# Optimization experiments

Hardware: AMD Instinct MI355X
Metric: run time of the kernel (lower is better)

Reference implementation:

```python
import jax, jax.numpy as jnp
import numpy as np

N, C = 8192, 256
CQK = C // 8  # q/k projection dim = 32


def setup_inputs() -> dict:
    key = jax.random.key(0)
    k1, k2, k3, k4, k5 = jax.random.split(key, 5)
    f = jax.random.normal(k1, (N, C), dtype=jnp.float32)
    Wqk = jax.random.normal(k2, (CQK, C), dtype=jnp.float32) * (1.0 / np.sqrt(C))
    Wv = jax.random.normal(k3, (C, C), dtype=jnp.float32) * (1.0 / np.sqrt(C))
    bv = jax.random.normal(k4, (C,), dtype=jnp.float32) * 0.01
    gamma = jax.random.normal(k5, (1,), dtype=jnp.float32)
    return {"f": f, "Wqk": Wqk, "Wv": Wv, "bv": bv, "gamma": gamma}


def reference(f, Wqk, Wv, bv, gamma):
    # f: [N, C] point features. 1x1 convs over the point dim == per-point linear.
    q = f @ Wqk.T                      # [N, CQK] (q and k share weights)
    # energy[i, j] = <q_i, k_j>; q == k here, no 1/sqrt(d) scaling (faithful)
    energy = q @ q.T                   # [N, N]
    attn = jax.nn.softmax(energy, axis=-1)  # softmax over last dim (dim=-1)
    v = f @ Wv.T + bv                  # [N, C]
    # torch: bmm(x_v [1,C,N], attn [1,N,N]) -> out[c, j] = sum_i v[i, c] * attn[i, j]
    attn_out = jnp.einsum('ij,ic->jc', attn, v)  # [N, C]
    return gamma[0] * attn_out + f     # [N, C]
```

## Files before the change

kernel.cpp:

```cpp
#include <hip/hip_runtime.h>
#include <hip/hip_bf16.h>

#define NN 8192
#define CC 256
#define CQK 32
#define JS 4

using bf16x8 = __attribute__((ext_vector_type(8))) short;
using f16x8  = __attribute__((ext_vector_type(8))) _Float16;
using s16x4  = __attribute__((ext_vector_type(4))) short;
using f32x4  = __attribute__((ext_vector_type(4))) float;
using f32x16 = __attribute__((ext_vector_type(16))) float;

static __device__ __forceinline__ unsigned short f2bf(float x) {
    union { __hip_bfloat16 h; unsigned short u; } cv;
    cv.h = __float2bfloat16(x);
    return cv.u;
}
static __device__ __forceinline__ float fexp2(float x) { return __builtin_amdgcn_exp2f(x); }
static __device__ __forceinline__ int packbf(float lo, float hi) {
    union { float f; unsigned u; } a, b;
    a.f = lo; b.f = hi;
    return (int)((b.u & 0xFFFF0000u) | (a.u >> 16));
}

__global__ __launch_bounds__(256) void conv_w_kernel(
    const float* __restrict__ Wv, unsigned short* __restrict__ WvB)
{
    const int idx = (blockIdx.x * 256 + threadIdx.x) * 4;
    float4 v = *(const float4*)(Wv + idx);
    s16x4 pk;
    pk[0] = (short)f2bf(v.x); pk[1] = (short)f2bf(v.y);
    pk[2] = (short)f2bf(v.z); pk[3] = (short)f2bf(v.w);
    *(s16x4*)(WvB + idx) = pk;
}

__global__ __launch_bounds__(256) void proj_q_kernel(
    const float* __restrict__ f, const float* __restrict__ Wqk,
    unsigned short* __restrict__ qf)
{
    __shared__ __align__(16) float fl[8][CC];
    const int t  = threadIdx.x;
    const int r0 = blockIdx.x * 8;
    {
        const float4* src = (const float4*)(f + (size_t)r0 * CC);
        float4* dst = (float4*)&fl[0][0];
        dst[t]       = src[t];
        dst[t + 256] = src[t + 256];
    }
    __syncthreads();
    const int cq = t & 31;
    const int rg = t >> 5;
    const float4* w4 = (const float4*)(Wqk + (size_t)cq * CC);
    float a = 0.f;
    for (int k4 = 0; k4 < 64; ++k4) {
        float4 wq = w4[k4];
        const float4 fv = *(const float4*)&fl[rg][k4 * 4];
        a = fmaf(wq.x, fv.x, a);
        a = fmaf(wq.y, fv.y, a);
        a = fmaf(wq.z, fv.z, a);
        a = fmaf(wq.w, fv.w, a);
    }
    a *= 1.2011224087864498f;
    union { _Float16 h; unsigned short u; } cv;
    cv.h = (_Float16)a;
    qf[(size_t)(r0 + rg) * CQK + cq] = cv.u;
}

__global__ __launch_bounds__(256, 4) void proj_v_kernel(
    const float* __restrict__ f, const unsigned short* __restrict__ WvB,
    const float* __restrict__ bv, unsigned short* __restrict__ vB)
{
    const int t    = threadIdx.x;
    const int lane = t & 63;
    const int w    = t >> 6;
    const int l31  = lane & 31;
    const int h    = lane >> 5;
    const int nb   = blockIdx.x * 32;
    const int cb   = w * 64;

    f32x16 acc[2];
#pragma unroll
    for (int cf = 0; cf < 2; ++cf)
#pragma unroll
        for (int r = 0; r < 16; ++r) acc[cf][r] = 0.f;

    const float* frow = f + (size_t)(nb + l31) * CC;
#pragma unroll
    for (int ks = 0; ks < 16; ++ks) {
        const int k0 = ks * 16 + 8 * h;
        float4 a0 = *(const float4*)(frow + k0);
        float4 a1 = *(const float4*)(frow + k0 + 4);
        bf16x8 af;
        af[0] = (short)f2bf(a0.x); af[1] = (short)f2bf(a0.y);
        af[2] = (short)f2bf(a0.z); af[3] = (short)f2bf(a0.w);
        af[4] = (short)f2bf(a1.x); af[5] = (short)f2bf(a1.y);
        af[6] = (short)f2bf(a1.z); af[7] = (short)f2bf(a1.w);
#pragma unroll
        for (int cf = 0; cf < 2; ++cf) {
            const bf16x8 bw = *(const bf16x8*)(WvB + (size_t)(cb + 32 * cf + l31) * CC + k0);
            acc[cf] = __builtin_amdgcn_mfma_f32_32x32x16_bf16(af, bw, acc[cf], 0, 0, 0);
        }
    }
#pragma unroll
    for (int cf = 0; cf < 2; ++cf) {
        const int cg = cb + 32 * cf + l31;
        const float bvc = bv[cg];
#pragma unroll
        for (int rg = 0; rg < 4; ++rg) {
            const int ib = (nb >> 3) + rg;
            s16x4 pk;
#pragma unroll
            for (int r = 0; r < 4; ++r)
                pk[r] = (short)f2bf(acc[cf][4 * rg + r] + bvc);
            *(s16x4*)(vB + ((size_t)ib * CC + cg) * 8 + 4 * h) = pk;
        }
    }
}

__global__ __launch_bounds__(256, 4) void pass1_kernel(
    const unsigned short* __restrict__ qf,
    float* __restrict__ ps)
{
    const int t    = threadIdx.x;
    const int lane = t & 63;
    const int w    = t >> 6;
    const int l31  = lane & 31;
    const int h    = lane >> 5;
    const int i0   = (blockIdx.x & 255) * 32;
    const int js   = blockIdx.x >> 8;
    const int JCH  = NN / JS / 4;
    const int jbase = js * (NN / JS) + w * JCH;

    const size_t qir = (size_t)(i0 + l31) * CQK;
    const f16x8 bi0 = *(const f16x8*)(qf + qir + 8 * h);
    const f16x8 bi1 = *(const f16x8*)(qf + qir + 16 + 8 * h);

    float s = 0.f;

#pragma unroll 2
    for (int st = 0; st < JCH; st += 32) {
        const size_t qjr = (size_t)(jbase + st + l31) * CQK;
        const f16x8 aj0 = *(const f16x8*)(qf + qjr + 8 * h);
        const f16x8 aj1 = *(const f16x8*)(qf + qjr + 16 + 8 * h);
        f32x16 ee = {0,0,0,0,0,0,0,0,0,0,0,0,0,0,0,0};
        ee = __builtin_amdgcn_mfma_f32_32x32x16_f16(aj0, bi0, ee, 0, 0, 0);
        ee = __builtin_amdgcn_mfma_f32_32x32x16_f16(aj1, bi1, ee, 0, 0, 0);
        float a_ = 0.f;
#pragma unroll
        for (int r = 0; r < 16; ++r) a_ += fexp2(ee[r]);
        s += a_;
    }
    s += __shfl_xor(s, 32);

    __shared__ float rs[4][32];
    if (lane < 32) rs[w][l31] = s;
    __syncthreads();
    if (t < 32) {
        float sf = rs[0][t] + rs[1][t] + rs[2][t] + rs[3][t];
        ps[(size_t)js * NN + i0 + t] = sf;
    }
}

__global__ __launch_bounds__(256) void finalize_kernel(
    const float* __restrict__ ps, float* __restrict__ bias)
{
    int i = blockIdx.x * 256 + threadIdx.x;
    float s = ps[i];
#pragma unroll
    for (int k = 1; k < JS; ++k) s += ps[(size_t)k * NN + i];
    bias[i] = __builtin_amdgcn_logf(s);
}

#define LOADQF(A0, A1, NI)                                                     \
    {                                                                          \
        const size_t qnr = (size_t)((NI) + l31) * CQK;                         \
        A0 = *(const f16x8*)(qf + qnr + 8 * h);                                \
        A1 = *(const f16x8*)(qf + qnr + 16 + 8 * h);                           \
    }

#define LOADVF2(VF, I)                                                         \
    _Pragma("unroll")                                                          \
    for (int s2 = 0; s2 < 2; ++s2)                                             \
        _Pragma("unroll")                                                      \
        for (int cf = 0; cf < 4; ++cf)                                         \
            VF[s2][cf] = *(const bf16x8*)(                                     \
                vB + ((size_t)(((I) >> 3) + 2 * s2 + h) * CC + cb + 32 * cf + l31) * 8);

#define LOADB42(B4, I)                                                         \
    _Pragma("unroll")                                                          \
    for (int rg = 0; rg < 4; ++rg)                                             \
        B4[rg] = *(const f32x4*)(bias + (I) + 8 * rg + 4 * h);

#define ECOMPF(EE, A0, A1)                                                     \
    {                                                                          \
        f32x16 z_ = {0,0,0,0,0,0,0,0,0,0,0,0,0,0,0,0};                         \
        z_ = __builtin_amdgcn_mfma_f32_32x32x16_f16(A1, bj1, z_, 0, 0, 0);     \
        EE = __builtin_amdgcn_mfma_f32_32x32x16_f16(A0, bj0, z_, 0, 0, 0);     \
    }

#define FINISH2(EE, B4, VF)                                                    \
    {                                                                          \
        int d0[4], d1[4];                                                      \
        _Pragma("unroll")                                                      \
        for (int rg = 0; rg < 4; ++rg) {                                       \
            float p0 = fexp2(EE[4 * rg + 0] - B4[rg][0]);                      \
            float p1 = fexp2(EE[4 * rg + 1] - B4[rg][1]);                      \
            float p2 = fexp2(EE[4 * rg + 2] - B4[rg][2]);                      \
            float p3 = fexp2(EE[4 * rg + 3] - B4[rg][3]);                      \
            d0[rg] = packbf(p0, p1);                                           \
            d1[rg] = packbf(p2, p3);                                           \
        }                                                                      \
        _Pragma("unroll")                                                      \
        for (int s2 = 0; s2 < 2; ++s2) {                                       \
            const int a_ = d0[2 * s2], b_ = d0[2 * s2 + 1];                    \
            const int c_ = d1[2 * s2], d_ = d1[2 * s2 + 1];                    \
            const int pa = __shfl_xor(a_, 32);                                 \
            const int pb = __shfl_xor(b_, 32);                                 \
            const int pc = __shfl_xor(c_, 32);                                 \
            const int pd = __shfl_xor(d_, 32);                                 \
            union { int i[4]; bf16x8 v; } pf;                                  \
            pf.i[0] = h ? pb : a_;                                             \
            pf.i[1] = h ? pd : c_;                                             \
            pf.i[2] = h ? b_ : pa;                                             \
            pf.i[3] = h ? d_ : pc;                                             \
            _Pragma("unroll")                                                  \
            for (int cf = 0; cf < 4; ++cf)                                     \
                acc[cf] = __builtin_amdgcn_mfma_f32_32x32x16_bf16(             \
                    pf.v, VF[s2][cf], acc[cf], 0, 0, 0);                       \
        }                                                                      \
    }

template<int ISPLIT, bool DIRECT>
__global__ __launch_bounds__(256, 2) void pass2_kernel(
    const unsigned short* __restrict__ qf,
    const unsigned short* __restrict__ vB,
    const float* __restrict__ bias,
    const float* __restrict__ f,
    const float* __restrict__ gp,
    float* __restrict__ dst)
{
    const int t    = threadIdx.x;
    const int lane = t & 63;
    const int w    = t >> 6;
    const int l31  = lane & 31;
    const int h    = lane >> 5;

    int jblk, isp;
    if (ISPLIT == 4) {
        const int bid = blockIdx.x;
        isp  = (bid & 7) >> 1;
        jblk = ((bid >> 3) << 1) | (bid & 1);
    } else if (ISPLIT == 2) {
        isp  = blockIdx.x & 1;
        jblk = blockIdx.x >> 1;
    } else {
        isp  = 0;
        jblk = blockIdx.x;
    }
    const int jb   = jblk * 64;
    const int jrow = jb + 32 * (w & 1);
    const int cb   = 128 * (w >> 1);
    const int IL   = NN / ISPLIT;
    const int ibase = isp * IL;
    const int iend  = ibase + IL;

    const size_t qjr = (size_t)(jrow + l31) * CQK;
    const f16x8 bj0 = *(const f16x8*)(qf + qjr + 8 * h);
    const f16x8 bj1 = *(const f16x8*)(qf + qjr + 16 + 8 * h);

    f32x16 acc[4];
#pragma unroll
    for (int cf = 0; cf < 4; ++cf)
#pragma unroll
        for (int r = 0; r < 16; ++r) acc[cf][r] = 0.f;

    f32x16 eeA, eeB;
    f32x4  b4A[4], b4B[4];
    f16x8  qa0, qa1, qb0, qb1;
    bf16x8 vfA[2][4], vfB[2][4];

    LOADQF(qa0, qa1, ibase)
    LOADB42(b4A, ibase)
    LOADVF2(vfA, ibase)
    ECOMPF(eeA, qa0, qa1)
    LOADQF(qb0, qb1, ibase + 32)
    LOADB42(b4B, ibase + 32)

    for (int i0s = ibase; i0s < iend; i0s += 64) {
        const int n1 = (i0s + 64 < iend) ? i0s + 64 : ibase;
        const int n2 = (i0s + 96 < iend) ? i0s + 96 : ibase;
        LOADVF2(vfB, i0s + 32)
        ECOMPF(eeB, qb0, qb1)
        LOADQF(qa0, qa1, n1)
        FINISH2(eeA, b4A, vfA)
        LOADB42(b4A, n1)
        LOADVF2(vfA, n1)
        ECOMPF(eeA, qa0, qa1)
        LOADQF(qb0, qb1, n2)
        FINISH2(eeB, b4B, vfB)
        LOADB42(b4B, n2)
    }

    if (DIRECT) {
        const float g = gp[0];
#pragma unroll
        for (int cf = 0; cf < 4; ++cf) {
            const int c = cb + 32 * cf + l31;
#pragma unroll
            for (int rg = 0; rg < 4; ++rg)
#pragma unroll
                for (int r = 0; r < 4; ++r) {
                    const int j = jrow + 4 * h + r + 8 * rg;
                    dst[(size_t)j * CC + c] =
                        fmaf(g, acc[cf][4 * rg + r], f[(size_t)j * CC + c]);
                }
        }
    } else {
        float* part = dst + (size_t)isp * NN * CC;
#pragma unroll
        for (int cf = 0; cf < 4; ++cf) {
            const int c = cb + 32 * cf + l31;
#pragma unroll
            for (int rg = 0; rg < 4; ++rg)
#pragma unroll
                for (int r = 0; r < 4; ++r) {
                    const int j = jrow + 4 * h + r + 8 * rg;
                    part[(size_t)j * CC + c] = acc[cf][4 * rg + r];
                }
        }
    }
}

template<int SPLIT>
__global__ __launch_bounds__(256) void reduce_kernel(
    const float* __restrict__ part, const float* __restrict__ f,
    const float* __restrict__ gp, float* __restrict__ out)
{
    size_t idx = (size_t)blockIdx.x * 256 + threadIdx.x;
    const f32x4* p4 = (const f32x4*)part;
    f32x4 s = p4[idx];
#pragma unroll
    for (int k = 1; k < SPLIT; ++k) s += p4[(size_t)k * (NN * CC / 4) + idx];
    f32x4 fv = ((const f32x4*)f)[idx];
    float g = gp[0];
    f32x4 o;
#pragma unroll
    for (int r = 0; r < 4; ++r) o[r] = fmaf(g, s[r], fv[r]);
    ((f32x4*)out)[idx] = o;
}

extern "C" void kernel_launch(void* const* d_in, const int* in_sizes, int n_in,
                              void* d_out, int out_size, void* d_ws, size_t ws_size,
                              hipStream_t stream) {
    const float* f     = (const float*)d_in[0];
    const float* Wqk   = (const float*)d_in[1];
    const float* Wv    = (const float*)d_in[2];
    const float* bv    = (const float*)d_in[3];
    const float* gamma = (const float*)d_in[4];
    float* out = (float*)d_out;

    char* ws = (char*)d_ws;
    unsigned short* qf  = (unsigned short*)ws;
    unsigned short* vB  = (unsigned short*)(ws + (1 << 20));
    float* ps   = (float*)(ws + (5 << 20));
    float* bias = (float*)(ws + (5 << 20) + (256 << 10));
    unsigned short* WvB = (unsigned short*)(ws + (5 << 20) + (512 << 10));
    float* part = (float*)(ws + (6 << 20));

    conv_w_kernel<<<dim3(CC * CC / 1024), dim3(256), 0, stream>>>(Wv, WvB);
    proj_q_kernel<<<dim3(NN / 8), dim3(256), 0, stream>>>(f, Wqk, qf);
    proj_v_kernel<<<dim3(NN / 32), dim3(256), 0, stream>>>(f, WvB, bv, vB);
    pass1_kernel<<<dim3((NN / 32) * JS), dim3(256), 0, stream>>>(qf, ps);
    finalize_kernel<<<dim3(NN / 256), dim3(256), 0, stream>>>(ps, bias);

    const size_t PB = (size_t)NN * CC * 4;
    const size_t B0 = (size_t)6 << 20;
    if (ws_size >= B0 + 4 * PB) {
        pass2_kernel<4, false><<<dim3(128 * 4), dim3(256), 0, stream>>>(qf, vB, bias, f, gamma, part);
        reduce_kernel<4><<<dim3(NN * CC / 1024), dim3(256), 0, stream>>>(part, f, gamma, out);
    } else if (ws_size >= B0 + 2 * PB) {
        pass2_kernel<2, false><<<dim3(128 * 2), dim3(256), 0, stream>>>(qf, vB, bias, f, gamma, part);
        reduce_kernel<2><<<dim3(NN * CC / 1024), dim3(256), 0, stream>>>(part, f, gamma, out);
    } else if (ws_size >= B0 + 1 * PB) {
        pass2_kernel<1, false><<<dim3(128), dim3(256), 0, stream>>>(qf, vB, bias, f, gamma, part);
        reduce_kernel<1><<<dim3(NN * CC / 1024), dim3(256), 0, stream>>>(part, f, gamma, out);
    } else {
        pass2_kernel<1, true><<<dim3(128), dim3(256), 0, stream>>>(qf, vB, bias, f, gamma, out);
    }
}
```

Measured before the change: 139.8 us.

## Give each wave all 256 channels, split i eightfold, store bf16 partials

Pass2 now assigns each wave 32 j-rows and all 256 output channels (8 accumulators) instead of 128 channels. Each exp/softmax tile is therefore computed once per j-row rather than twice, and the QK energy MFMAs are halved. The i-range split rises to 8 to keep enough blocks in flight. Partial sums are stored as bf16 to halve partial write/read traffic, and V fragments are loaded inline rather than prefetched. The trade-offs are higher register pressure from 128 accumulator floats at launch bounds 2, exposed V load latency, and a precision loss from rounding partials to bf16.

Result: slower. 234.6 us (+67.7%).

```diff
diff --git a/kernel.cpp b/kernel.cpp
--- a/kernel.cpp
+++ b/kernel.cpp
@@ -16,6 +16,11 @@
     union { __hip_bfloat16 h; unsigned short u; } cv;
     cv.h = __float2bfloat16(x);
     return cv.u;
+}
+static __device__ __forceinline__ float bf2f(unsigned short u) {
+    union { unsigned u; float f; } cv;
+    cv.u = (unsigned)u << 16;
+    return cv.f;
 }
 static __device__ __forceinline__ float fexp2(float x) { return __builtin_amdgcn_exp2f(x); }
 static __device__ __forceinline__ int packbf(float lo, float hi) {
@@ -179,15 +184,7 @@
         A1 = *(const f16x8*)(qf + qnr + 16 + 8 * h);                           \
     }
 
-#define LOADVF2(VF, I)                                                         \
-    _Pragma("unroll")                                                          \
-    for (int s2 = 0; s2 < 2; ++s2)                                             \
-        _Pragma("unroll")                                                      \
-        for (int cf = 0; cf < 4; ++cf)                                         \
-            VF[s2][cf] = *(const bf16x8*)(                                     \
-                vB + ((size_t)(((I) >> 3) + 2 * s2 + h) * CC + cb + 32 * cf + l31) * 8);
-
-#define LOADB42(B4, I)                                                         \
+#define LOADB4S(B4, I)                                                         \
     _Pragma("unroll")                                                          \
     for (int rg = 0; rg < 4; ++rg)                                             \
         B4[rg] = *(const f32x4*)(bias + (I) + 8 * rg + 4 * h);
@@ -199,7 +196,7 @@
         EE = __builtin_amdgcn_mfma_f32_32x32x16_f16(A0, bj0, z_, 0, 0, 0);     \
     }
 
-#define FINISH2(EE, B4, VF)                                                    \
+#define FINISH_R1(EE, B4, IG)                                                  \
     {                                                                          \
         int d0[4], d1[4];                                                      \
         _Pragma("unroll")                                                      \
@@ -224,10 +221,13 @@
             pf.i[1] = h ? pd : c_;                                             \
             pf.i[2] = h ? b_ : pa;                                             \
             pf.i[3] = h ? d_ : pc;                                             \
+            const size_t vbase = ((size_t)(((IG) >> 3) + 2 * s2 + h) * CC + l31) * 8; \
             _Pragma("unroll")                                                  \
-            for (int cf = 0; cf < 4; ++cf)                                     \
+            for (int cf = 0; cf < 8; ++cf) {                                   \
+                const bf16x8 vf = *(const bf16x8*)(vB + vbase + (size_t)cf * 256); \
                 acc[cf] = __builtin_amdgcn_mfma_f32_32x32x16_bf16(             \
-                    pf.v, VF[s2][cf], acc[cf], 0, 0, 0);                       \
+                    pf.v, vf, acc[cf], 0, 0, 0);                               \
+            }                                                                  \
         }                                                                      \
     }
 
@@ -238,7 +238,7 @@
     const float* __restrict__ bias,
     const float* __restrict__ f,
     const float* __restrict__ gp,
-    float* __restrict__ dst)
+    void* __restrict__ dstv)
 {
     const int t    = threadIdx.x;
     const int lane = t & 63;
@@ -247,7 +247,10 @@
     const int h    = lane >> 5;
 
     int jblk, isp;
-    if (ISPLIT == 4) {
+    if (ISPLIT == 8) {
+        isp  = blockIdx.x & 7;
+        jblk = blockIdx.x >> 3;
+    } else if (ISPLIT == 4) {
         const int bid = blockIdx.x;
         isp  = (bid & 7) >> 1;
         jblk = ((bid >> 3) << 1) | (bid & 1);
@@ -258,9 +261,7 @@
         isp  = 0;
         jblk = blockIdx.x;
     }
-    const int jb   = jblk * 64;
-    const int jrow = jb + 32 * (w & 1);
-    const int cb   = 128 * (w >> 1);
+    const int jrow = jblk * 128 + 32 * w;
     const int IL   = NN / ISPLIT;
     const int ibase = isp * IL;
     const int iend  = ibase + IL;
@@ -269,44 +270,39 @@
     const f16x8 bj0 = *(const f16x8*)(qf + qjr + 8 * h);
     const f16x8 bj1 = *(const f16x8*)(qf + qjr + 16 + 8 * h);
 
-    f32x16 acc[4];
-#pragma unroll
-    for (int cf = 0; cf < 4; ++cf)
+    f32x16 acc[8];
+#pragma unroll
+    for (int cf = 0; cf < 8; ++cf)
 #pragma unroll
         for (int r = 0; r < 16; ++r) acc[cf][r] = 0.f;
 
     f32x16 eeA, eeB;
-    f32x4  b4A[4], b4B[4];
+    f32x4  b4[4];
     f16x8  qa0, qa1, qb0, qb1;
-    bf16x8 vfA[2][4], vfB[2][4];
 
     LOADQF(qa0, qa1, ibase)
-    LOADB42(b4A, ibase)
-    LOADVF2(vfA, ibase)
     ECOMPF(eeA, qa0, qa1)
     LOADQF(qb0, qb1, ibase + 32)
-    LOADB42(b4B, ibase + 32)
 
     for (int i0s = ibase; i0s < iend; i0s += 64) {
         const int n1 = (i0s + 64 < iend) ? i0s + 64 : ibase;
         const int n2 = (i0s + 96 < iend) ? i0s + 96 : ibase;
-        LOADVF2(vfB, i0s + 32)
+        LOADB4S(b4, i0s)
         ECOMPF(eeB, qb0, qb1)
         LOADQF(qa0, qa1, n1)
-        FINISH2(eeA, b4A, vfA)
-        LOADB42(b4A, n1)
-        LOADVF2(vfA, n1)
+        FINISH_R1(eeA, b4, i0s)
+        LOADB4S(b4, i0s + 32)
         ECOMPF(eeA, qa0, qa1)
         LOADQF(qb0, qb1, n2)
-        FINISH2(eeB, b4B, vfB)
-        LOADB42(b4B, n2)
+        FINISH_R1(eeB, b4, i0s + 32)
     }
 
     if (DIRECT) {
+        float* dst = (float*)dstv;
         const float g = gp[0];
 #pragma unroll
-        for (int cf = 0; cf < 4; ++cf) {
-            const int c = cb + 32 * cf + l31;
+        for (int cf = 0; cf < 8; ++cf) {
+            const int c = 32 * cf + l31;
 #pragma unroll
             for (int rg = 0; rg < 4; ++rg)
 #pragma unroll
@@ -317,16 +313,16 @@
                 }
         }
     } else {
-        float* part = dst + (size_t)isp * NN * CC;
-#pragma unroll
-        for (int cf = 0; cf < 4; ++cf) {
-            const int c = cb + 32 * cf + l31;
+        unsigned short* part = (unsigned short*)dstv + (size_t)isp * NN * CC;
+#pragma unroll
+        for (int cf = 0; cf < 8; ++cf) {
+            const int c = 32 * cf + l31;
 #pragma unroll
             for (int rg = 0; rg < 4; ++rg)
 #pragma unroll
                 for (int r = 0; r < 4; ++r) {
                     const int j = jrow + 4 * h + r + 8 * rg;
-                    part[(size_t)j * CC + c] = acc[cf][4 * rg + r];
+                    part[(size_t)j * CC + c] = f2bf(acc[cf][4 * rg + r]);
                 }
         }
     }
@@ -334,19 +330,26 @@
 
 template<int SPLIT>
 __global__ __launch_bounds__(256) void reduce_kernel(
-    const float* __restrict__ part, const float* __restrict__ f,
+    const unsigned short* __restrict__ part, const float* __restrict__ f,
     const float* __restrict__ gp, float* __restrict__ out)
 {
     size_t idx = (size_t)blockIdx.x * 256 + threadIdx.x;
-    const f32x4* p4 = (const f32x4*)part;
-    f32x4 s = p4[idx];
-#pragma unroll
-    for (int k = 1; k < SPLIT; ++k) s += p4[(size_t)k * (NN * CC / 4) + idx];
-    f32x4 fv = ((const f32x4*)f)[idx];
-    float g = gp[0];
+    float s0 = 0.f, s1 = 0.f, s2 = 0.f, s3 = 0.f;
+#pragma unroll
+    for (int k = 0; k < SPLIT; ++k) {
+        const s16x4 v = *(const s16x4*)(part + (size_t)k * NN * CC + idx * 4);
+        s0 += bf2f((unsigned short)v[0]);
+        s1 += bf2f((unsigned short)v[1]);
+        s2 += bf2f((unsigned short)v[2]);
+        s3 += bf2f((unsigned short)v[3]);
+    }
+    const f32x4 fv = ((const f32x4*)f)[idx];
+    const float g = gp[0];
     f32x4 o;
-#pragma unroll
-    for (int r = 0; r < 4; ++r) o[r] = fmaf(g, s[r], fv[r]);
+    o[0] = fmaf(g, s0, fv[0]);
+    o[1] = fmaf(g, s1, fv[1]);
+    o[2] = fmaf(g, s2, fv[2]);
+    o[3] = fmaf(g, s3, fv[3]);
     ((f32x4*)out)[idx] = o;
 }
 
@@ -366,7 +369,7 @@
     float* ps   = (float*)(ws + (5 << 20));
     float* bias = (float*)(ws + (5 << 20) + (256 << 10));
     unsigned short* WvB = (unsigned short*)(ws + (5 << 20) + (512 << 10));
-    float* part = (float*)(ws + (6 << 20));
+    unsigned short* part = (unsigned short*)(ws + (6 << 20));
 
     conv_w_kernel<<<dim3(CC * CC / 1024), dim3(256), 0, stream>>>(Wv, WvB);
     proj_q_kernel<<<dim3(NN / 8), dim3(256), 0, stream>>>(f, Wqk, qf);
@@ -374,18 +377,18 @@
     pass1_kernel<<<dim3((NN / 32) * JS), dim3(256), 0, stream>>>(qf, ps);
     finalize_kernel<<<dim3(NN / 256), dim3(256), 0, stream>>>(ps, bias);
 
-    const size_t PB = (size_t)NN * CC * 4;
+    const size_t PB = (size_t)NN * CC * 2;
     const size_t B0 = (size_t)6 << 20;
-    if (ws_size >= B0 + 4 * PB) {
-        pass2_kernel<4, false><<<dim3(128 * 4), dim3(256), 0, stream>>>(qf, vB, bias, f, gamma, part);
+    if (ws_size >= B0 + 8 * PB) {
+        pass2_kernel<8, false><<<dim3(64 * 8), dim3(256), 0, stream>>>(qf, vB, bias, f, gamma, part);
+        reduce_kernel<8><<<dim3(NN * CC / 1024), dim3(256), 0, stream>>>(part, f, gamma, out);
+    } else if (ws_size >= B0 + 4 * PB) {
+        pass2_kernel<4, false><<<dim3(64 * 4), dim3(256), 0, stream>>>(qf, vB, bias, f, gamma, part);
         reduce_kernel<4><<<dim3(NN * CC / 1024), dim3(256), 0, stream>>>(part, f, gamma, out);
     } else if (ws_size >= B0 + 2 * PB) {
-        pass2_kernel<2, false><<<dim3(128 * 2), dim3(256), 0, stream>>>(qf, vB, bias, f, gamma, part);
+        pass2_kernel<2, false><<<dim3(64 * 2), dim3(256), 0, stream>>>(qf, vB, bias, f, gamma, part);
         reduce_kernel<2><<<dim3(NN * CC / 1024), dim3(256), 0, stream>>>(part, f, gamma, out);
-    } else if (ws_size >= B0 + 1 * PB) {
-        pass2_kernel<1, false><<<dim3(128), dim3(256), 0, stream>>>(qf, vB, bias, f, gamma, part);
-        reduce_kernel<1><<<dim3(NN * CC / 1024), dim3(256), 0, stream>>>(part, f, gamma, out);
     } else {
-        pass2_kernel<1, true><<<dim3(128), dim3(256), 0, stream>>>(qf, vB, bias, f, gamma, out);
-    }
-}
+        pass2_kernel<1, true><<<dim3(64), dim3(256), 0, stream>>>(qf, vB, bias, f, gamma, out);
+    }
+}
```

## Merge projection kernels and store split-i partials as bf16

Applied to the files above, without the earlier changes.

Folds the Wv conversion, q projection and v projection into one launch. The v branch now converts Wv to bf16 inline instead of reading a pre-converted copy. The pass2 partial sums are written as bf16 instead of fp32, halving the traffic for partial writes and reduce reads, and the SPLIT=1 non-direct path is dropped. This cuts launch overhead and memory traffic at the cost of lower precision in the partial accumulations, plus redundant Wv conversion in every v block.

Result: faster. 133.7 us (-4.4%).

```diff
diff --git a/kernel.cpp b/kernel.cpp
--- a/kernel.cpp
+++ b/kernel.cpp
@@ -17,6 +17,11 @@
     cv.h = __float2bfloat16(x);
     return cv.u;
 }
+static __device__ __forceinline__ float bf2f(unsigned short u) {
+    union { unsigned u; float f; } cv;
+    cv.u = (unsigned)u << 16;
+    return cv.f;
+}
 static __device__ __forceinline__ float fexp2(float x) { return __builtin_amdgcn_exp2f(x); }
 static __device__ __forceinline__ int packbf(float lo, float hi) {
     union { float f; unsigned u; } a, b;
@@ -24,96 +29,90 @@
     return (int)((b.u & 0xFFFF0000u) | (a.u >> 16));
 }
 
-__global__ __launch_bounds__(256) void conv_w_kernel(
-    const float* __restrict__ Wv, unsigned short* __restrict__ WvB)
-{
-    const int idx = (blockIdx.x * 256 + threadIdx.x) * 4;
-    float4 v = *(const float4*)(Wv + idx);
-    s16x4 pk;
-    pk[0] = (short)f2bf(v.x); pk[1] = (short)f2bf(v.y);
-    pk[2] = (short)f2bf(v.z); pk[3] = (short)f2bf(v.w);
-    *(s16x4*)(WvB + idx) = pk;
-}
-
-__global__ __launch_bounds__(256) void proj_q_kernel(
+__global__ __launch_bounds__(256) void proj_kernel(
     const float* __restrict__ f, const float* __restrict__ Wqk,
-    unsigned short* __restrict__ qf)
+    const float* __restrict__ Wv, const float* __restrict__ bv,
+    unsigned short* __restrict__ qf, unsigned short* __restrict__ vB)
 {
     __shared__ __align__(16) float fl[8][CC];
-    const int t  = threadIdx.x;
-    const int r0 = blockIdx.x * 8;
-    {
-        const float4* src = (const float4*)(f + (size_t)r0 * CC);
-        float4* dst = (float4*)&fl[0][0];
-        dst[t]       = src[t];
-        dst[t + 256] = src[t + 256];
-    }
-    __syncthreads();
-    const int cq = t & 31;
-    const int rg = t >> 5;
-    const float4* w4 = (const float4*)(Wqk + (size_t)cq * CC);
-    float a = 0.f;
-    for (int k4 = 0; k4 < 64; ++k4) {
-        float4 wq = w4[k4];
-        const float4 fv = *(const float4*)&fl[rg][k4 * 4];
-        a = fmaf(wq.x, fv.x, a);
-        a = fmaf(wq.y, fv.y, a);
-        a = fmaf(wq.z, fv.z, a);
-        a = fmaf(wq.w, fv.w, a);
-    }
-    a *= 1.2011224087864498f;
-    union { _Float16 h; unsigned short u; } cv;
-    cv.h = (_Float16)a;
-    qf[(size_t)(r0 + rg) * CQK + cq] = cv.u;
-}
-
-__global__ __launch_bounds__(256, 4) void proj_v_kernel(
-    const float* __restrict__ f, const unsigned short* __restrict__ WvB,
-    const float* __restrict__ bv, unsigned short* __restrict__ vB)
-{
-    const int t    = threadIdx.x;
-    const int lane = t & 63;
-    const int w    = t >> 6;
-    const int l31  = lane & 31;
-    const int h    = lane >> 5;
-    const int nb   = blockIdx.x * 32;
-    const int cb   = w * 64;
-
-    f32x16 acc[2];
-#pragma unroll
-    for (int cf = 0; cf < 2; ++cf)
-#pragma unroll
-        for (int r = 0; r < 16; ++r) acc[cf][r] = 0.f;
-
-    const float* frow = f + (size_t)(nb + l31) * CC;
-#pragma unroll
-    for (int ks = 0; ks < 16; ++ks) {
-        const int k0 = ks * 16 + 8 * h;
-        float4 a0 = *(const float4*)(frow + k0);
-        float4 a1 = *(const float4*)(frow + k0 + 4);
-        bf16x8 af;
-        af[0] = (short)f2bf(a0.x); af[1] = (short)f2bf(a0.y);
-        af[2] = (short)f2bf(a0.z); af[3] = (short)f2bf(a0.w);
-        af[4] = (short)f2bf(a1.x); af[5] = (short)f2bf(a1.y);
-        af[6] = (short)f2bf(a1.z); af[7] = (short)f2bf(a1.w);
+    const int t = threadIdx.x;
+
+    if (blockIdx.x < 1024) {
+        const int r0 = blockIdx.x * 8;
+        {
+            const float4* src = (const float4*)(f + (size_t)r0 * CC);
+            float4* dst = (float4*)&fl[0][0];
+            dst[t]       = src[t];
+            dst[t + 256] = src[t + 256];
+        }
+        __syncthreads();
+        const int cq = t & 31;
+        const int rg = t >> 5;
+        const float4* w4 = (const float4*)(Wqk + (size_t)cq * CC);
+        float a = 0.f;
+        for (int k4 = 0; k4 < 64; ++k4) {
+            float4 wq = w4[k4];
+            const float4 fv = *(const float4*)&fl[rg][k4 * 4];
+            a = fmaf(wq.x, fv.x, a);
+            a = fmaf(wq.y, fv.y, a);
+            a = fmaf(wq.z, fv.z, a);
+            a = fmaf(wq.w, fv.w, a);
+        }
+        a *= 1.2011224087864498f;
+        union { _Float16 h; unsigned short u; } cv;
+        cv.h = (_Float16)a;
+        qf[(size_t)(r0 + rg) * CQK + cq] = cv.u;
+    } else {
+        const int lane = t & 63;
+        const int w    = t >> 6;
+        const int l31  = lane & 31;
+        const int h    = lane >> 5;
+        const int nb   = (blockIdx.x - 1024) * 32;
+        const int cb   = w * 64;
+
+        f32x16 acc[2];
+#pragma unroll
+        for (int cf = 0; cf < 2; ++cf)
+#pragma unroll
+            for (int r = 0; r < 16; ++r) acc[cf][r] = 0.f;
+
+        const float* frow = f + (size_t)(nb + l31) * CC;
+#pragma unroll
+        for (int ks = 0; ks < 16; ++ks) {
+            const int k0 = ks * 16 + 8 * h;
+            float4 a0 = *(const float4*)(frow + k0);
+            float4 a1 = *(const float4*)(frow + k0 + 4);
+            bf16x8 af;
+            af[0] = (short)f2bf(a0.x); af[1] = (short)f2bf(a0.y);
+            af[2] = (short)f2bf(a0.z); af[3] = (short)f2bf(a0.w);
+            af[4] = (short)f2bf(a1.x); af[5] = (short)f2bf(a1.y);
+            af[6] = (short)f2bf(a1.z); af[7] = (short)f2bf(a1.w);
+#pragma unroll
+            for (int cf = 0; cf < 2; ++cf) {
+                const float* wrow = Wv + (size_t)(cb + 32 * cf + l31) * CC + k0;
+                float4 b0 = *(const float4*)(wrow);
+                float4 b1 = *(const float4*)(wrow + 4);
+                bf16x8 bw;
+                bw[0] = (short)f2bf(b0.x); bw[1] = (short)f2bf(b0.y);
+                bw[2] = (short)f2bf(b0.z); bw[3] = (short)f2bf(b0.w);
+                bw[4] = (short)f2bf(b1.x); bw[5] = (short)f2bf(b1.y);
+                bw[6] = (short)f2bf(b1.z); bw[7] = (short)f2bf(b1.w);
+                acc[cf] = __builtin_amdgcn_mfma_f32_32x32x16_bf16(af, bw, acc[cf], 0, 0, 0);
+            }
+        }
 #pragma unroll
         for (int cf = 0; cf < 2; ++cf) {
-            const bf16x8 bw = *(const bf16x8*)(WvB + (size_t)(cb + 32 * cf + l31) * CC + k0);
-            acc[cf] = __builtin_amdgcn_mfma_f32_32x32x16_bf16(af, bw, acc[cf], 0, 0, 0);
-        }
-    }
-#pragma unroll
-    for (int cf = 0; cf < 2; ++cf) {
-        const int cg = cb + 32 * cf + l31;
-        const float bvc = bv[cg];
-#pragma unroll
-        for (int rg = 0; rg < 4; ++rg) {
-            const int ib = (nb >> 3) + rg;
-            s16x4 pk;
-#pragma unroll
-            for (int r = 0; r < 4; ++r)
-                pk[r] = (short)f2bf(acc[cf][4 * rg + r] + bvc);
-            *(s16x4*)(vB + ((size_t)ib * CC + cg) * 8 + 4 * h) = pk;
+            const int cg = cb + 32 * cf + l31;
+            const float bvc = bv[cg];
+#pragma unroll
+            for (int rg = 0; rg < 4; ++rg) {
+                const int ib = (nb >> 3) + rg;
+                s16x4 pk;
+#pragma unroll
+                for (int r = 0; r < 4; ++r)
+                    pk[r] = (short)f2bf(acc[cf][4 * rg + r] + bvc);
+                *(s16x4*)(vB + ((size_t)ib * CC + cg) * 8 + 4 * h) = pk;
+            }
         }
     }
 }
@@ -238,7 +237,7 @@
     const float* __restrict__ bias,
     const float* __restrict__ f,
     const float* __restrict__ gp,
-    float* __restrict__ dst)
+    void* __restrict__ dstv)
 {
     const int t    = threadIdx.x;
     const int lane = t & 63;
@@ -303,6 +302,7 @@
     }
 
     if (DIRECT) {
+        float* dst = (float*)dstv;
         const float g = gp[0];
 #pragma unroll
         for (int cf = 0; cf < 4; ++cf) {
@@ -317,7 +317,7 @@
                 }
         }
     } else {
-        float* part = dst + (size_t)isp * NN * CC;
+        unsigned short* part = (unsigned short*)dstv + (size_t)isp * NN * CC;
 #pragma unroll
         for (int cf = 0; cf < 4; ++cf) {
             const int c = cb + 32 * cf + l31;
@@ -326,7 +326,7 @@
 #pragma unroll
                 for (int r = 0; r < 4; ++r) {
                     const int j = jrow + 4 * h + r + 8 * rg;
-                    part[(size_t)j * CC + c] = acc[cf][4 * rg + r];
+                    part[(size_t)j * CC + c] = f2bf(acc[cf][4 * rg + r]);
                 }
         }
     }
@@ -334,19 +334,26 @@
 
 template<int SPLIT>
 __global__ __launch_bounds__(256) void reduce_kernel(
-    const float* __restrict__ part, const float* __restrict__ f,
+    const unsigned short* __restrict__ part, const float* __restrict__ f,
     const float* __restrict__ gp, float* __restrict__ out)
 {
     size_t idx = (size_t)blockIdx.x * 256 + threadIdx.x;
-    const f32x4* p4 = (const f32x4*)part;
-    f32x4 s = p4[idx];
-#pragma unroll
-    for (int k = 1; k < SPLIT; ++k) s += p4[(size_t)k * (NN * CC / 4) + idx];
-    f32x4 fv = ((const f32x4*)f)[idx];
-    float g = gp[0];
+    float s0 = 0.f, s1 = 0.f, s2 = 0.f, s3 = 0.f;
+#pragma unroll
+    for (int k = 0; k < SPLIT; ++k) {
+        const s16x4 v = *(const s16x4*)(part + (size_t)k * NN * CC + idx * 4);
+        s0 += bf2f((unsigned short)v[0]);
+        s1 += bf2f((unsigned short)v[1]);
+        s2 += bf2f((unsigned short)v[2]);
+        s3 += bf2f((unsigned short)v[3]);
+    }
+    const f32x4 fv = ((const f32x4*)f)[idx];
+    const float g = gp[0];
     f32x4 o;
-#pragma unroll
-    for (int r = 0; r < 4; ++r) o[r] = fmaf(g, s[r], fv[r]);
+    o[0] = fmaf(g, s0, fv[0]);
+    o[1] = fmaf(g, s1, fv[1]);
+    o[2] = fmaf(g, s2, fv[2]);
+    o[3] = fmaf(g, s3, fv[3]);
     ((f32x4*)out)[idx] = o;
 }
 
@@ -365,16 +372,13 @@
     unsigned short* vB  = (unsigned short*)(ws + (1 << 20));
     float* ps   = (float*)(ws + (5 << 20));
     float* bias = (float*)(ws + (5 << 20) + (256 << 10));
-    unsigned short* WvB = (unsigned short*)(ws + (5 << 20) + (512 << 10));
-    float* part = (float*)(ws + (6 << 20));
-
-    conv_w_kernel<<<dim3(CC * CC / 1024), dim3(256), 0, stream>>>(Wv, WvB);
-    proj_q_kernel<<<dim3(NN / 8), dim3(256), 0, stream>>>(f, Wqk, qf);
-    proj_v_kernel<<<dim3(NN / 32), dim3(256), 0, stream>>>(f, WvB, bv, vB);
+    unsigned short* part = (unsigned short*)(ws + (6 << 20));
+
+    proj_kernel<<<dim3(1024 + NN / 32), dim3(256), 0, stream>>>(f, Wqk, Wv, bv, qf, vB);
     pass1_kernel<<<dim3((NN / 32) * JS), dim3(256), 0, stream>>>(qf, ps);
     finalize_kernel<<<dim3(NN / 256), dim3(256), 0, stream>>>(ps, bias);
 
-    const size_t PB = (size_t)NN * CC * 4;
+    const size_t PB = (size_t)NN * CC * 2;
     const size_t B0 = (size_t)6 << 20;
     if (ws_size >= B0 + 4 * PB) {
         pass2_kernel<4, false><<<dim3(128 * 4), dim3(256), 0, stream>>>(qf, vB, bias, f, gamma, part);
@@ -382,9 +386,6 @@
     } else if (ws_size >= B0 + 2 * PB) {
         pass2_kernel<2, false><<<dim3(128 * 2), dim3(256), 0, stream>>>(qf, vB, bias, f, gamma, part);
         reduce_kernel<2><<<dim3(NN * CC / 1024), dim3(256), 0, stream>>>(part, f, gamma, out);
-    } else if (ws_size >= B0 + 1 * PB) {
-        pass2_kernel<1, false><<<dim3(128), dim3(256), 0, stream>>>(qf, vB, bias, f, gamma, part);
-        reduce_kernel<1><<<dim3(NN * CC / 1024), dim3(256), 0, stream>>>(part, f, gamma, out);
     } else {
         pass2_kernel<1, true><<<dim3(128), dim3(256), 0, stream>>>(qf, vB, bias, f, gamma, out);
     }
```
